# Performance work log

Hardware: AMD Instinct MI355X
Metric: run time of the kernel (lower is better)

Reference implementation:

```python
import jax, jax.numpy as jnp
import numpy as np

J = 24  # fixed pooling window (SampleLength/N = 1200/50)


def setup_inputs() -> dict:
    key = jax.random.key(0)
    k1, k2, k3 = jax.random.split(key, 3)
    T, N, K, C = 786432, 50, 400, 10  # T = 32768 segments * J
    x = jax.random.normal(k1, (T, N), dtype=jnp.float32)
    W1 = jax.random.normal(k2, (K, N), dtype=jnp.float32) * 0.1
    W2 = jax.random.normal(k3, (C, K), dtype=jnp.float32) * 0.1
    return {"x": x, "W1": W1, "W2": W2}


def reference(x, W1, W2):
    # linear + relu: [T, N] @ [N, K] -> [T, K]
    local_features = jax.nn.relu(jnp.einsum('tn,kn->tk', x, W1))
    # fixed-window mean over consecutive J rows: [T, K] -> [T//J, K]
    T, K = local_features.shape
    features = local_features.reshape(T // J, J, K).mean(axis=1)
    # final linear: [T//J, K] @ [K, C] -> [T//J, C]
    logits = jnp.einsum('bk,ck->bc', features, W2)
    return logits
```

## Files before the change

kernel.cpp:

```cpp
#include <hip/hip_runtime.h>
#include <hip/hip_bf16.h>

#define T_TOTAL 786432
#define N_IN 50
#define K_FEAT 400
#define C_OUT 10
#define NSEG 32768

#define W1F_TASKS (25 * 2 * 64)
#define W2T_OFF_BYTES 51200
#define W2T_FLOATS (25 * 320)
#define W2F_OFF_BYTES 83200
#define W2F_TASKS (13 * 64)
#define PREP_TASKS (W1F_TASKS + W2T_FLOATS + W2F_TASKS)
#define POOLED_OFF_BYTES 98304
#define POOLED_STRIDE 416
#define WS_NEEDED (POOLED_OFF_BYTES + (size_t)NSEG * POOLED_STRIDE * 2)

typedef __bf16 bfx8 __attribute__((ext_vector_type(8)));
typedef short  s16x8 __attribute__((ext_vector_type(8)));
typedef float  f32x4 __attribute__((ext_vector_type(4)));

static __device__ __forceinline__ short f2bf(float f) {
    union { float f; unsigned u; } v; v.f = f;
    unsigned r = v.u + 0x7fffu + ((v.u >> 16) & 1u);
    return (short)(r >> 16);
}

__global__ void prep_kernel(const float* __restrict__ W1,
                            const float* __restrict__ W2,
                            short* __restrict__ w1f, float* __restrict__ w2t,
                            short* __restrict__ w2f)
{
    const int gid = blockIdx.x * blockDim.x + threadIdx.x;
    if (gid < W1F_TASKS) {
        const int lane = gid & 63;
        const int s    = (gid >> 6) & 1;
        const int tile = gid >> 7;
        const int m16  = lane & 15;
        const int quad = lane >> 4;
        const float* row = W1 + (tile * 16 + m16) * N_IN;
        s16x8 v;
        #pragma unroll
        for (int j = 0; j < 8; ++j) {
            const int n = s * 32 + quad * 8 + j;
            v[j] = (n < N_IN) ? f2bf(row[n]) : (short)0;
        }
        *(s16x8*)&w1f[gid * 8] = v;
    } else if (gid < W1F_TASKS + W2T_FLOATS) {
        const int i   = gid - W1F_TASKS;
        const int j   = i / 320;
        const int tid = i - j * 320;
        const int o    = tid >> 4;
        const int part = tid & 15;
        const int seg  = (o >= 10) ? 1 : 0;
        const int cls  = o - seg * 10;
        w2t[i] = W2[cls * K_FEAT + part * 25 + j];
    } else if (gid < PREP_TASKS) {
        const int i    = gid - W1F_TASKS - W2T_FLOATS;
        const int lane = i & 63;
        const int kt   = i >> 6;
        const int m16  = lane & 15;
        const int quad = lane >> 4;
        s16x8 v;
        #pragma unroll
        for (int j = 0; j < 8; ++j) {
            const int feat = kt * 32 + quad * 8 + j;
            v[j] = (m16 < C_OUT && feat < K_FEAT) ? f2bf(W2[m16 * K_FEAT + feat])
                                                  : (short)0;
        }
        *(s16x8*)&w2f[i * 8] = v;
    }
}

__global__ __launch_bounds__(256, 3) void phase1_kernel(
    const float* __restrict__ x, const short* __restrict__ w1f,
    short* __restrict__ pooled)
{
    const int tid  = threadIdx.x;
    const int wave = tid >> 6;
    const int lane = tid & 63;
    const int m16  = lane & 15;
    const int quad = lane >> 4;
    const int wgid = blockIdx.x * 4 + wave;
    const s16x8* wf = (const s16x8*)w1f;

    for (int g = 0; g < 2; ++g) {
        const int group = wgid * 2 + g;
        const float* xg = x + (size_t)group * (2 * 48 * N_IN);

        s16x8 A[6][2];
        #pragma unroll
        for (int ct = 0; ct < 6; ++ct) {
            const float* rp = xg + (ct * 16 + m16) * N_IN;
            float v0[8], v1[8];
            #pragma unroll
            for (int h = 0; h < 4; ++h) {
                const float2 u = *(const float2*)(rp + quad * 8 + 2 * h);
                v0[2 * h] = u.x; v0[2 * h + 1] = u.y;
            }
            if (quad < 2) {
                #pragma unroll
                for (int h = 0; h < 4; ++h) {
                    const float2 u = *(const float2*)(rp + 32 + quad * 8 + 2 * h);
                    v1[2 * h] = u.x; v1[2 * h + 1] = u.y;
                }
            } else if (quad == 2) {
                const float2 u = *(const float2*)(rp + 48);
                v1[0] = u.x; v1[1] = u.y;
                #pragma unroll
                for (int j = 2; j < 8; ++j) v1[j] = 0.f;
            } else {
                #pragma unroll
                for (int j = 0; j < 8; ++j) v1[j] = 0.f;
            }
            s16x8 f0, f1;
            #pragma unroll
            for (int j = 0; j < 8; ++j) { f0[j] = f2bf(v0[j]); f1[j] = f2bf(v1[j]); }
            A[ct][0] = f0; A[ct][1] = f1;
        }

        s16x8 b0 = wf[lane];
        s16x8 b1 = wf[64 + lane];
        const int seg0 = group * 4;
        for (int t = 0; t < 25; ++t) {
            const int tn = (t < 24) ? t + 1 : 24;
            const s16x8 nb0 = wf[(tn * 2) * 64 + lane];
            const s16x8 nb1 = wf[(tn * 2 + 1) * 64 + lane];
            #pragma unroll
            for (int h = 0; h < 2; ++h) {
                float c0 = 0.f, c1 = 0.f;
                #pragma unroll
                for (int r = 0; r < 3; ++r) {
                    f32x4 acc = {0.f, 0.f, 0.f, 0.f};
                    acc = __builtin_amdgcn_mfma_f32_16x16x32_bf16(
                            __builtin_bit_cast(bfx8, A[h * 3 + r][0]),
                            __builtin_bit_cast(bfx8, b0), acc, 0, 0, 0);
                    acc = __builtin_amdgcn_mfma_f32_16x16x32_bf16(
                            __builtin_bit_cast(bfx8, A[h * 3 + r][1]),
                            __builtin_bit_cast(bfx8, b1), acc, 0, 0, 0);
                    const float s = fmaxf(acc[0], 0.f) + fmaxf(acc[1], 0.f)
                                  + fmaxf(acc[2], 0.f) + fmaxf(acc[3], 0.f);
                    if (r * 4 + quad < 6) c0 += s; else c1 += s;
                }
                c0 += __shfl_xor(c0, 16); c0 += __shfl_xor(c0, 32);
                c1 += __shfl_xor(c1, 16); c1 += __shfl_xor(c1, 32);
                if (quad < 2) {
                    const int seg = seg0 + 2 * h + quad;
                    const float cv = (quad == 0) ? c0 : c1;
                    pooled[(size_t)seg * POOLED_STRIDE + t * 16 + m16] = f2bf(cv);
                }
            }
            b0 = nb0; b1 = nb1;
        }
    }
}

__global__ __launch_bounds__(256) void phase2_kernel(
    const short* __restrict__ pooled, const short* __restrict__ w2f,
    float* __restrict__ out)
{
    const int tid  = threadIdx.x;
    const int lane = tid & 63;
    const int m16  = lane & 15;
    const int quad = lane >> 4;
    const int segbase = (blockIdx.x * 4 + (tid >> 6)) * 16;
    const s16x8* wf = (const s16x8*)w2f;
    const short* arow = pooled + (size_t)(segbase + m16) * POOLED_STRIDE;

    f32x4 acc = {0.f, 0.f, 0.f, 0.f};
    s16x8 zero = {0, 0, 0, 0, 0, 0, 0, 0};
    #pragma unroll
    for (int kt = 0; kt < 13; ++kt) {
        const s16x8 b = wf[kt * 64 + lane];
        const s16x8 a = (kt == 12 && quad >= 2)
                            ? zero
                            : *(const s16x8*)(arow + kt * 32 + quad * 8);
        acc = __builtin_amdgcn_mfma_f32_16x16x32_bf16(
                __builtin_bit_cast(bfx8, a), __builtin_bit_cast(bfx8, b),
                acc, 0, 0, 0);
    }
    if (m16 < C_OUT) {
        #pragma unroll
        for (int rg = 0; rg < 4; ++rg)
            out[(size_t)(segbase + quad * 4 + rg) * C_OUT + m16] =
                acc[rg] * (1.0f / 24.0f);
    }
}

#define FB_CPB 4
#define FB_NTHREADS 320
#define FB_XS_STRIDE 72
#define FB_XS_ROWS (FB_CPB * 48)

__global__ __launch_bounds__(FB_NTHREADS) void classifier_fb(
    const float* __restrict__ x, const short* __restrict__ w1f,
    const float* __restrict__ w2t, float* __restrict__ out)
{
    __shared__ short xs[FB_XS_ROWS * FB_XS_STRIDE];
    __shared__ float pooled[2 * K_FEAT];

    const int tid  = threadIdx.x;
    const int wave = tid >> 6;
    const int lane = tid & 63;
    const int m16  = lane & 15;
    const int quad = lane >> 4;

    {
        const float* xb = x + (size_t)blockIdx.x * (FB_XS_ROWS * N_IN);
        #pragma unroll
        for (int it = 0; it < (FB_XS_ROWS * 25) / FB_NTHREADS; ++it) {
            const int i = tid + it * FB_NTHREADS;
            const int r = i / 25;
            const int c2 = i - r * 25;
            const float2 v = *(const float2*)(xb + 2 * i);
            const int packed = (unsigned short)f2bf(v.x) |
                               ((unsigned)(unsigned short)f2bf(v.y) << 16);
            *(int*)&xs[r * FB_XS_STRIDE + 2 * c2] = packed;
        }
        for (int i = tid; i < FB_XS_ROWS * 7; i += FB_NTHREADS) {
            const int r = i / 7;
            const int c = 50 + 2 * (i - r * 7);
            *(int*)&xs[r * FB_XS_STRIDE + c] = 0;
        }
    }

    s16x8 bfrag[5][2];
    {
        const s16x8* wf = (const s16x8*)w1f;
        #pragma unroll
        for (int t = 0; t < 5; ++t)
            #pragma unroll
            for (int s = 0; s < 2; ++s)
                bfrag[t][s] = wf[((wave * 5 + t) * 2 + s) * 64 + lane];
    }

    const int o    = tid >> 4;
    const int part = tid & 15;
    const int segO = (o >= 10) ? 1 : 0;
    const int cls  = o - segO * 10;
    float w2r[25];
    #pragma unroll
    for (int j = 0; j < 25; ++j) w2r[j] = w2t[j * FB_NTHREADS + tid];

    __syncthreads();

    for (int ciq = 0; ciq < FB_CPB; ++ciq) {
        s16x8 a[3][2];
        #pragma unroll
        for (int r = 0; r < 3; ++r) {
            const short* arow =
                &xs[(ciq * 48 + r * 16 + m16) * FB_XS_STRIDE + quad * 8];
            a[r][0] = *(const s16x8*)(arow);
            a[r][1] = *(const s16x8*)(arow + 32);
        }
        #pragma unroll
        for (int t = 0; t < 5; ++t) {
            float c0 = 0.f, c1 = 0.f;
            #pragma unroll
            for (int r = 0; r < 3; ++r) {
                f32x4 acc = {0.f, 0.f, 0.f, 0.f};
                acc = __builtin_amdgcn_mfma_f32_16x16x32_bf16(
                        __builtin_bit_cast(bfx8, a[r][0]),
                        __builtin_bit_cast(bfx8, bfrag[t][0]), acc, 0, 0, 0);
                acc = __builtin_amdgcn_mfma_f32_16x16x32_bf16(
                        __builtin_bit_cast(bfx8, a[r][1]),
                        __builtin_bit_cast(bfx8, bfrag[t][1]), acc, 0, 0, 0);
                const float s = fmaxf(acc[0], 0.f) + fmaxf(acc[1], 0.f)
                              + fmaxf(acc[2], 0.f) + fmaxf(acc[3], 0.f);
                if (r * 4 + quad < 6) c0 += s; else c1 += s;
            }
            c0 += __shfl_xor(c0, 16); c0 += __shfl_xor(c0, 32);
            c1 += __shfl_xor(c1, 16); c1 += __shfl_xor(c1, 32);
            if (quad == 0) {
                const int feat = (wave * 5 + t) * 16 + m16;
                pooled[feat] = c0;
                pooled[K_FEAT + feat] = c1;
            }
        }
        __syncthreads();

        float sum = 0.f;
        const float* pv = &pooled[segO * K_FEAT + part * 25];
        #pragma unroll
        for (int j = 0; j < 25; ++j) sum += pv[j] * w2r[j];
        sum += __shfl_down(sum, 8, 16);
        sum += __shfl_down(sum, 4, 16);
        sum += __shfl_down(sum, 2, 16);
        sum += __shfl_down(sum, 1, 16);
        if (part == 0) {
            const int chunk = blockIdx.x * FB_CPB + ciq;
            out[(chunk * 2 + segO) * C_OUT + cls] = sum * (1.0f / 24.0f);
        }
        __syncthreads();
    }
}

extern "C" void kernel_launch(void* const* d_in, const int* in_sizes, int n_in,
                              void* d_out, int out_size, void* d_ws, size_t ws_size,
                              hipStream_t stream) {
    const float* x  = (const float*)d_in[0];
    const float* W1 = (const float*)d_in[1];
    const float* W2 = (const float*)d_in[2];
    float* out = (float*)d_out;

    short* w1f = (short*)d_ws;
    float* w2t = (float*)((char*)d_ws + W2T_OFF_BYTES);
    short* w2f = (short*)((char*)d_ws + W2F_OFF_BYTES);
    short* pooled = (short*)((char*)d_ws + POOLED_OFF_BYTES);

    prep_kernel<<<(PREP_TASKS + 255) / 256, 256, 0, stream>>>(W1, W2, w1f, w2t, w2f);

    if (ws_size >= WS_NEEDED) {
        phase1_kernel<<<1024, 256, 0, stream>>>(x, w1f, pooled);
        phase2_kernel<<<512, 256, 0, stream>>>(pooled, w2f, out);
    } else {
        classifier_fb<<<4096, FB_NTHREADS, 0, stream>>>(x, w1f, w2t, out);
    }
}
```

Before: 289.5 us.

## Switch phase1 GEMM to 32x32x16 MFMA tiles with new W1 fragment layout

Phase1 now uses 32x32x16 bf16 MFMA instead of 16x16x32. Each wave processes 96 rows (four segments) against 32-feature tiles, so the loop runs 13 times instead of 25 and each step needs fewer pooling shuffles. Prep gains a new W1 fragment layout padded to 416 features and 64 input columns, which moves the pooled buffer's workspace offset. Each wave now handles one group instead of two, so the grid doubles to 2048 blocks and launch bounds rise to 4 waves. The price is padding waste in both K (50 to 64) and features (400 to 416), plus larger accumulator register pressure.

```diff
diff --git a/kernel.cpp b/kernel.cpp
--- a/kernel.cpp
+++ b/kernel.cpp
@@ -12,14 +12,17 @@
 #define W2T_FLOATS (25 * 320)
 #define W2F_OFF_BYTES 83200
 #define W2F_TASKS (13 * 64)
-#define PREP_TASKS (W1F_TASKS + W2T_FLOATS + W2F_TASKS)
-#define POOLED_OFF_BYTES 98304
+#define W1F32_OFF_BYTES 98304
+#define W1F32_TASKS (13 * 4 * 64)
+#define PREP_TASKS (W1F_TASKS + W2T_FLOATS + W2F_TASKS + W1F32_TASKS)
+#define POOLED_OFF_BYTES 163840
 #define POOLED_STRIDE 416
 #define WS_NEEDED (POOLED_OFF_BYTES + (size_t)NSEG * POOLED_STRIDE * 2)
 
 typedef __bf16 bfx8 __attribute__((ext_vector_type(8)));
 typedef short  s16x8 __attribute__((ext_vector_type(8)));
 typedef float  f32x4 __attribute__((ext_vector_type(4)));
+typedef float  f32x16 __attribute__((ext_vector_type(16)));
 
 static __device__ __forceinline__ short f2bf(float f) {
     union { float f; unsigned u; } v; v.f = f;
@@ -30,7 +33,7 @@
 __global__ void prep_kernel(const float* __restrict__ W1,
                             const float* __restrict__ W2,
                             short* __restrict__ w1f, float* __restrict__ w2t,
-                            short* __restrict__ w2f)
+                            short* __restrict__ w2f, short* __restrict__ w1f32)
 {
     const int gid = blockIdx.x * blockDim.x + threadIdx.x;
     if (gid < W1F_TASKS) {
@@ -56,7 +59,7 @@
         const int seg  = (o >= 10) ? 1 : 0;
         const int cls  = o - seg * 10;
         w2t[i] = W2[cls * K_FEAT + part * 25 + j];
-    } else if (gid < PREP_TASKS) {
+    } else if (gid < W1F_TASKS + W2T_FLOATS + W2F_TASKS) {
         const int i    = gid - W1F_TASKS - W2T_FLOATS;
         const int lane = i & 63;
         const int kt   = i >> 6;
@@ -70,89 +73,108 @@
                                                   : (short)0;
         }
         *(s16x8*)&w2f[i * 8] = v;
-    }
-}
-
-__global__ __launch_bounds__(256, 3) void phase1_kernel(
-    const float* __restrict__ x, const short* __restrict__ w1f,
+    } else if (gid < PREP_TASKS) {
+        const int i    = gid - W1F_TASKS - W2T_FLOATS - W2F_TASKS;
+        const int lane = i & 63;
+        const int fi   = i >> 6;
+        const int ft   = fi >> 2;
+        const int kt   = fi & 3;
+        const int feat = ft * 32 + (lane & 31);
+        const int cbase = kt * 16 + (lane >> 5) * 8;
+        s16x8 v;
+        #pragma unroll
+        for (int j = 0; j < 8; ++j) {
+            const int col = cbase + j;
+            v[j] = (feat < K_FEAT && col < N_IN) ? f2bf(W1[feat * N_IN + col])
+                                                 : (short)0;
+        }
+        *(s16x8*)&w1f32[i * 8] = v;
+    }
+}
+
+__global__ __launch_bounds__(256, 4) void phase1_kernel(
+    const float* __restrict__ x, const short* __restrict__ w1f32,
     short* __restrict__ pooled)
 {
     const int tid  = threadIdx.x;
-    const int wave = tid >> 6;
     const int lane = tid & 63;
-    const int m16  = lane & 15;
-    const int quad = lane >> 4;
-    const int wgid = blockIdx.x * 4 + wave;
-    const s16x8* wf = (const s16x8*)w1f;
-
-    for (int g = 0; g < 2; ++g) {
-        const int group = wgid * 2 + g;
-        const float* xg = x + (size_t)group * (2 * 48 * N_IN);
-
-        s16x8 A[6][2];
-        #pragma unroll
-        for (int ct = 0; ct < 6; ++ct) {
-            const float* rp = xg + (ct * 16 + m16) * N_IN;
-            float v0[8], v1[8];
-            #pragma unroll
-            for (int h = 0; h < 4; ++h) {
-                const float2 u = *(const float2*)(rp + quad * 8 + 2 * h);
-                v0[2 * h] = u.x; v0[2 * h + 1] = u.y;
-            }
-            if (quad < 2) {
+    const int m32  = lane & 31;
+    const int h    = lane >> 5;
+    const int chunk = blockIdx.x * 4 + (tid >> 6);
+    const s16x8* wf = (const s16x8*)w1f32;
+
+    s16x8 Af[3][4];
+    {
+        const float* xg = x + (size_t)chunk * (96 * N_IN);
+        #pragma unroll
+        for (int rt = 0; rt < 3; ++rt) {
+            const float* rp = xg + (32 * rt + m32) * N_IN;
+            #pragma unroll
+            for (int kt = 0; kt < 3; ++kt) {
+                const float* p = rp + 16 * kt + 8 * h;
+                s16x8 f;
                 #pragma unroll
-                for (int h = 0; h < 4; ++h) {
-                    const float2 u = *(const float2*)(rp + 32 + quad * 8 + 2 * h);
-                    v1[2 * h] = u.x; v1[2 * h + 1] = u.y;
+                for (int q = 0; q < 4; ++q) {
+                    const float2 u = *(const float2*)(p + 2 * q);
+                    f[2 * q]     = f2bf(u.x);
+                    f[2 * q + 1] = f2bf(u.y);
                 }
-            } else if (quad == 2) {
+                Af[rt][kt] = f;
+            }
+            s16x8 f3 = {0, 0, 0, 0, 0, 0, 0, 0};
+            if (h == 0) {
                 const float2 u = *(const float2*)(rp + 48);
-                v1[0] = u.x; v1[1] = u.y;
-                #pragma unroll
-                for (int j = 2; j < 8; ++j) v1[j] = 0.f;
-            } else {
-                #pragma unroll
-                for (int j = 0; j < 8; ++j) v1[j] = 0.f;
-            }
-            s16x8 f0, f1;
-            #pragma unroll
-            for (int j = 0; j < 8; ++j) { f0[j] = f2bf(v0[j]); f1[j] = f2bf(v1[j]); }
-            A[ct][0] = f0; A[ct][1] = f1;
-        }
-
-        s16x8 b0 = wf[lane];
-        s16x8 b1 = wf[64 + lane];
-        const int seg0 = group * 4;
-        for (int t = 0; t < 25; ++t) {
-            const int tn = (t < 24) ? t + 1 : 24;
-            const s16x8 nb0 = wf[(tn * 2) * 64 + lane];
-            const s16x8 nb1 = wf[(tn * 2 + 1) * 64 + lane];
-            #pragma unroll
-            for (int h = 0; h < 2; ++h) {
-                float c0 = 0.f, c1 = 0.f;
-                #pragma unroll
-                for (int r = 0; r < 3; ++r) {
-                    f32x4 acc = {0.f, 0.f, 0.f, 0.f};
-                    acc = __builtin_amdgcn_mfma_f32_16x16x32_bf16(
-                            __builtin_bit_cast(bfx8, A[h * 3 + r][0]),
-                            __builtin_bit_cast(bfx8, b0), acc, 0, 0, 0);
-                    acc = __builtin_amdgcn_mfma_f32_16x16x32_bf16(
-                            __builtin_bit_cast(bfx8, A[h * 3 + r][1]),
-                            __builtin_bit_cast(bfx8, b1), acc, 0, 0, 0);
-                    const float s = fmaxf(acc[0], 0.f) + fmaxf(acc[1], 0.f)
-                                  + fmaxf(acc[2], 0.f) + fmaxf(acc[3], 0.f);
-                    if (r * 4 + quad < 6) c0 += s; else c1 += s;
-                }
-                c0 += __shfl_xor(c0, 16); c0 += __shfl_xor(c0, 32);
-                c1 += __shfl_xor(c1, 16); c1 += __shfl_xor(c1, 32);
-                if (quad < 2) {
-                    const int seg = seg0 + 2 * h + quad;
-                    const float cv = (quad == 0) ? c0 : c1;
-                    pooled[(size_t)seg * POOLED_STRIDE + t * 16 + m16] = f2bf(cv);
-                }
-            }
-            b0 = nb0; b1 = nb1;
-        }
+                f3[0] = f2bf(u.x); f3[1] = f2bf(u.y);
+            }
+            Af[rt][3] = f3;
+        }
+    }
+
+    const int segbase = chunk * 4;
+
+    s16x8 Bc[4], Bn[4];
+    #pragma unroll
+    for (int kt = 0; kt < 4; ++kt) Bc[kt] = wf[kt * 64 + lane];
+
+    for (int ft = 0; ft < 13; ++ft) {
+        const int ftn = (ft < 12) ? ft + 1 : 12;
+        #pragma unroll
+        for (int kt = 0; kt < 4; ++kt) Bn[kt] = wf[(ftn * 4 + kt) * 64 + lane];
+
+        float s0 = 0.f, s1 = 0.f, s2 = 0.f, s3 = 0.f;
+        #pragma unroll
+        for (int rt = 0; rt < 3; ++rt) {
+            f32x16 acc;
+            #pragma unroll
+            for (int r = 0; r < 16; ++r) acc[r] = 0.f;
+            #pragma unroll
+            for (int kt = 0; kt < 4; ++kt)
+                acc = __builtin_amdgcn_mfma_f32_32x32x16_bf16(
+                        __builtin_bit_cast(bfx8, Af[rt][kt]),
+                        __builtin_bit_cast(bfx8, Bc[kt]), acc, 0, 0, 0);
+            float c0 = 0.f, c1 = 0.f;
+            #pragma unroll
+            for (int r = 0; r < 16; ++r) {
+                const float v = fmaxf(acc[r], 0.f);
+                if ((r >> 2) < 3 - rt) c0 += v; else c1 += v;
+            }
+            if (rt == 0)      { s0 += c0; s1 += c1; }
+            else if (rt == 1) { s1 += c0; s2 += c1; }
+            else              { s2 += c0; s3 += c1; }
+        }
+        s0 += __shfl_xor(s0, 32);
+        s1 += __shfl_xor(s1, 32);
+        s2 += __shfl_xor(s2, 32);
+        s3 += __shfl_xor(s3, 32);
+        if (lane < 32) {
+            const size_t fo = 32 * ft + lane;
+            pooled[(size_t)(segbase + 0) * POOLED_STRIDE + fo] = f2bf(s0);
+            pooled[(size_t)(segbase + 1) * POOLED_STRIDE + fo] = f2bf(s1);
+            pooled[(size_t)(segbase + 2) * POOLED_STRIDE + fo] = f2bf(s2);
+            pooled[(size_t)(segbase + 3) * POOLED_STRIDE + fo] = f2bf(s3);
+        }
+        #pragma unroll
+        for (int kt = 0; kt < 4; ++kt) Bc[kt] = Bn[kt];
     }
 }
 
@@ -304,15 +326,17 @@
     const float* W2 = (const float*)d_in[2];
     float* out = (float*)d_out;
 
-    short* w1f = (short*)d_ws;
-    float* w2t = (float*)((char*)d_ws + W2T_OFF_BYTES);
-    short* w2f = (short*)((char*)d_ws + W2F_OFF_BYTES);
+    short* w1f   = (short*)d_ws;
+    float* w2t   = (float*)((char*)d_ws + W2T_OFF_BYTES);
+    short* w2f   = (short*)((char*)d_ws + W2F_OFF_BYTES);
+    short* w1f32 = (short*)((char*)d_ws + W1F32_OFF_BYTES);
     short* pooled = (short*)((char*)d_ws + POOLED_OFF_BYTES);
 
-    prep_kernel<<<(PREP_TASKS + 255) / 256, 256, 0, stream>>>(W1, W2, w1f, w2t, w2f);
+    prep_kernel<<<(PREP_TASKS + 255) / 256, 256, 0, stream>>>(W1, W2, w1f, w2t,
+                                                              w2f, w1f32);
 
     if (ws_size >= WS_NEEDED) {
-        phase1_kernel<<<1024, 256, 0, stream>>>(x, w1f, pooled);
+        phase1_kernel<<<2048, 256, 0, stream>>>(x, w1f32, pooled);
         phase2_kernel<<<512, 256, 0, stream>>>(pooled, w2f, out);
     } else {
         classifier_fb<<<4096, FB_NTHREADS, 0, stream>>>(x, w1f, w2t, out);
```

New measurement: 262.8 us. 1.1x faster.
